# Performance work log

Hardware: AMD Instinct MI355X
Metric: run time of the kernel (lower is better)

Reference implementation:

```python
import jax, jax.numpy as jnp
import numpy as np
import math

HIDDEN = 32
N_NODES = 4096
N_EDGES = 8192
FEAT = HIDDEN * 16
# e3nn FullyConnectedTensorProduct instruction order: loop i_in1, i_in2, i_out
PATHS = [(l1, l2, l3) for l1 in range(4) for l2 in range(4) for l3 in range(4)
         if abs(l1 - l2) <= l3 <= l1 + l2 and (l1 + l2 + l3) % 2 == 0]
WEIGHT_NUMEL = len(PATHS) * HIDDEN * HIDDEN  # 23 * 1024 = 23552
_CNT = {l3: sum(1 for p in PATHS if p[2] == l3) for l3 in range(4)}
# path_weight: irrep_normalization='component', path_normalization='element'
PATH_W = {p: math.sqrt((2 * p[2] + 1) / (_CNT[p[2]] * HIDDEN)) for p in PATHS}


def _sh(xp, x, y, z):
    # e3nn-convention real spherical harmonics l=0..3, 'component' normalization.
    # Assumes unit-norm (x,y,z). xp is np or jnp.
    s3, s5, s7, s15 = math.sqrt(3.), math.sqrt(5.), math.sqrt(7.), math.sqrt(15.)
    c58, c38 = math.sqrt(5. / 8.), math.sqrt(3. / 8.)
    comps = [
        xp.ones_like(x),
        s3 * x, s3 * y, s3 * z,
        s5 * s3 * x * z, s5 * s3 * x * y, s5 * (y * y - 0.5 * (x * x + z * z)),
        s5 * s3 * y * z, s5 * (s3 / 2.) * (z * z - x * x),
        s7 * c58 * x * (3. * z * z - x * x), s7 * s15 * x * y * z,
        s7 * c38 * x * (5. * y * y - 1.), s7 * 0.5 * y * (5. * y * y - 3.),
        s7 * c38 * z * (5. * y * y - 1.), s7 * (s15 / 2.) * y * (z * z - x * x),
        s7 * c58 * z * (z * z - 3. * x * x),
    ]
    return xp.stack(comps, axis=-1)


def _wigner_tables():
    # Real-basis unit-Frobenius invariant tensors (e3nn wigner_3j up to sign),
    # computed as Gaunt integrals of the real SH over the sphere (exact quadrature:
    # integrand degree <= 9, Gauss-Legendre x uniform phi).
    nu, nphi = 16, 32
    u, wu = np.polynomial.legendre.leggauss(nu)
    phi = np.arange(nphi) * (2.0 * np.pi / nphi)
    uu = np.repeat(u, nphi)
    ww = np.repeat(wu, nphi) * (2.0 * np.pi / nphi)
    pp = np.tile(phi, nu)
    st = np.sqrt(np.maximum(1.0 - uu * uu, 0.0))
    Y = _sh(np, st * np.cos(pp), st * np.sin(pp), uu)  # [P,16]
    tabs = {}
    for key in set(PATHS):
        l1, l2, l3 = key
        C = np.einsum('p,pi,pj,pk->ijk', ww,
                      Y[:, l1 * l1:(l1 + 1) ** 2],
                      Y[:, l2 * l2:(l2 + 1) ** 2],
                      Y[:, l3 * l3:(l3 + 1) ** 2])
        tabs[key] = (C / np.linalg.norm(C)).astype(np.float32)
    return tabs


W3J = _wigner_tables()


def setup_inputs():
    key = jax.random.key(0)
    k1, k2, k3, k4, k5 = jax.random.split(key, 5)
    return {
        'node_features': jax.random.normal(k1, (N_NODES, FEAT), jnp.float32),
        'edge_index': jax.random.randint(k2, (2, N_EDGES), 0, N_NODES),
        'edge_vectors': jax.random.normal(k3, (N_EDGES, 3), jnp.float32),
        'w_weight': jax.random.uniform(k4, (WEIGHT_NUMEL, 1), jnp.float32, -1.0, 1.0),
        'w_bias': jax.random.uniform(k5, (WEIGHT_NUMEL,), jnp.float32, -1.0, 1.0),
    }


def reference(node_features, edge_index, edge_vectors, w_weight, w_bias):
    src, dst = edge_index[0], edge_index[1]
    N = node_features.shape[0]
    E = edge_vectors.shape[0]
    lengths = jnp.maximum(jnp.linalg.norm(edge_vectors, axis=-1, keepdims=True), 1e-8)
    unit = edge_vectors / lengths
    Y = _sh(jnp, unit[:, 0], unit[:, 1], unit[:, 2])            # [E,16]
    # weight_net: Linear(1, weight_numel)
    W = lengths * w_weight[:, 0][None, :] + w_bias[None, :]     # [E,23552]
    x_src = node_features[src]                                  # [E,512] gather
    acc = [jnp.zeros((E, HIDDEN, 2 * l + 1), node_features.dtype) for l in range(4)]
    for p_idx, (l1, l2, l3) in enumerate(PATHS):
        x1 = x_src[:, HIDDEN * l1 * l1: HIDDEN * (l1 + 1) ** 2].reshape(E, HIDDEN, 2 * l1 + 1)
        y2 = Y[:, l2 * l2:(l2 + 1) ** 2]                        # [E,2l2+1]
        C = jnp.asarray(W3J[(l1, l2, l3)])                      # [2l1+1,2l2+1,2l3+1]
        wp = W[:, p_idx * HIDDEN * HIDDEN:(p_idx + 1) * HIDDEN * HIDDEN].reshape(E, HIDDEN, HIDDEN)
        tmp = jnp.einsum('eui,ej,ijk->euk', x1, y2, C)
        acc[l3] = acc[l3] + PATH_W[(l1, l2, l3)] * jnp.einsum('euk,euw->ewk', tmp, wp)
    messages = jnp.concatenate([a.reshape(E, -1) for a in acc], axis=-1)  # [E,512]
    return jax.ops.segment_sum(messages, dst, num_segments=N)
```

## Files before the change

kernel.cpp:

```cpp
#include <hip/hip_runtime.h>
#include <math.h>

#define N_PATHS 23
#define HIDDEN  32
#define N_NODES 4096
#define N_EDGES 8192
#define FEAT    512
#define BLK     128
#define ZERO_BLOCKS 256

#define WAVE_SYNC() asm volatile("s_waitcnt lgkmcnt(0)" ::: "memory")

typedef __attribute__((ext_vector_type(8)))  short bf16x8;
typedef __attribute__((ext_vector_type(16))) float f32x16;

constexpr int cL1[N_PATHS] = {0,0,0,0, 1,1,1,1,1,1, 2,2,2,2,2,2,2, 3,3,3,3,3,3};
constexpr int cL2[N_PATHS] = {0,1,2,3, 0,1,1,2,2,3, 0,1,1,2,2,3,3, 0,1,2,2,3,3};
constexpr int cCOFF[N_PATHS]= {0,1,10,35,84,93,102,147,192,297,402,427,472,577,602,727,832,1077,1126,1231,1336,1581,1630};
constexpr int cL3P[N_PATHS] = {0,5,13,21, 1,4,7,11,15,19, 2,6,9,10,14,18,22, 3,8,12,16,17,20};
constexpr int cL3S[5] = {0,4,10,17,23};
constexpr int cOFF3[4] = {0,32,128,288};
__device__ const int CNT_L3[4] = {4,6,7,6};
__device__ const int D_L3[N_PATHS] = {0,1,2,3, 1,0,2,1,3,2, 2,1,3,0,2,1,3, 3,2,1,3,0,2};

constexpr int zOff(int G, int pi) {
    int off = 0;
    for (int q = cL3S[G]; q < pi; ++q) off += (2*cL1[cL3P[q]]+1)*(2*G+1);
    return off;
}

__device__ const double GLX8[8] = {
    -0.96028985649753623168, -0.79666647741362673959, -0.52553240991632898582, -0.18343464249564980494,
     0.18343464249564980494,  0.52553240991632898582,  0.79666647741362673959,  0.96028985649753623168};
__device__ const double GLW8[8] = {
     0.10122853629037625915,  0.22238103445337447054,  0.31370664587788728734,  0.36268378337836198297,
     0.36268378337836198297,  0.31370664587788728734,  0.22238103445337447054,  0.10122853629037625915};
__device__ const double COSP16[16] = {
  1.0,                     0.92387953251128675613,  0.70710678118654752440,  0.38268343236508977173,
  0.0,                    -0.38268343236508977173, -0.70710678118654752440, -0.92387953251128675613,
 -1.0,                    -0.92387953251128675613, -0.70710678118654752440, -0.38268343236508977173,
  0.0,                     0.38268343236508977173,  0.70710678118654752440,  0.92387953251128675613};
__device__ const double SINP16[16] = {
  0.0,                     0.38268343236508977173,  0.70710678118654752440,  0.92387953251128675613,
  1.0,                     0.92387953251128675613,  0.70710678118654752440,  0.38268343236508977173,
  0.0,                    -0.38268343236508977173, -0.70710678118654752440, -0.92387953251128675613,
 -1.0,                    -0.92387953251128675613, -0.70710678118654752440, -0.38268343236508977173};

__device__ inline void sh_f64(double x, double y, double z, double* Y) {
    const double s3 = 1.7320508075688772935, s5 = 2.2360679774997896964,
                 s7 = 2.6457513110645905905, s15 = 3.8729833462074168852;
    const double c58 = 0.79056941504209483300, c38 = 0.61237243569579452455;
    Y[0] = 1.0;
    Y[1] = s3*x;  Y[2] = s3*y;  Y[3] = s3*z;
    Y[4] = s5*s3*x*z;  Y[5] = s5*s3*x*y;
    Y[6] = s5*(y*y - 0.5*(x*x + z*z));
    Y[7] = s5*s3*y*z;  Y[8] = s5*(s3/2.0)*(z*z - x*x);
    Y[9] = s7*c58*x*(3.0*z*z - x*x);
    Y[10]= s7*s15*x*y*z;
    Y[11]= s7*c38*x*(5.0*y*y - 1.0);
    Y[12]= s7*0.5*y*(5.0*y*y - 3.0);
    Y[13]= s7*c38*z*(5.0*y*y - 1.0);
    Y[14]= s7*(s15/2.0)*y*(z*z - x*x);
// ... 88 lines not shown
        float acc = 0.f;
        if (entry < csize) {
            const int i = entry/(d2*d3); const int r = entry - i*(d2*d3);
            const int j = r/d3; const int k = r - j*d3;
            const int ai = l1*l1+i, bi = l2*l2+j, ci = l3*l3+k;
#pragma unroll 4
            for (int it = 0; it < 32; ++it) {
                const int q = it*4 + sub;
                acc = fmaf(s_wq[q] * s_Yq[q][ai] * s_Yq[q][bi], s_Yq[q][ci], acc);
            }
        }
        acc += __shfl_xor(acc, 1);
        acc += __shfl_xor(acc, 2);
        if (sub == 0 && entry < csize) s_part[entry] = acc;
    }
    __syncthreads();

    if (t < 256) { const float v = (t < csize) ? s_part[t] : 0.f; red[t] = v*v; }
    __syncthreads();
    for (int s = 128; s > 0; s >>= 1) {
        if (t < s) red[t] += red[t+s];
        __syncthreads();
    }
    if (t == 0) {
        const float pw = sqrtf((float)(2*l3+1) / ((float)CNT_L3[l3] * (float)HIDDEN));
        s_scale = pw / sqrtf(red[0]);
    }
    __syncthreads();
    if (t < csize) g_w3j[cCOFF[p] + t] = s_part[t] * s_scale;
}

template<int G, int P, int ZOFF>
__device__ __forceinline__ void do_zpath(
    int lane, const float* __restrict__ w3j, const float* sY, float* sz)
{
    constexpr int l1 = cL1[P], l2 = cL2[P];
    constexpr int d1 = 2*l1+1, d2 = 2*l2+1, d3 = 2*G+1;
    constexpr int zc = d1*d3;
#pragma unroll
    for (int base = 0; base < 4*zc; base += 64) {
        const int idx = base + lane;
        if (idx < 4*zc) {
            const int elz = idx / zc;
            const int r = idx - elz*zc;
            const int i = r / d3, k = r - i*d3;
            const float* Cp = w3j + cCOFF[P] + i*(d2*d3) + k;
            const float* Yp = sY + elz*16 + l2*l2;
            float acc = 0.f;
#pragma unroll
            for (int j = 0; j < d2; ++j) acc = fmaf(Yp[j], Cp[j*d3], acc);
            sz[4*ZOFF + elz*zc + r] = acc;
        }
    }
}

template<int G, int P, int ZOFF>
__device__ __forceinline__ void do_path(
    int lane, int el4, int u0, int bvaddr, int avaddr,
    const float (&xr0)[16], const float (&xr1)[16],
    const unsigned short* __restrict__ Awhi, const unsigned short* __restrict__ Awlo,
    const unsigned short* __restrict__ Abhi, const unsigned short* __restrict__ Ablo,
    const float* sz,
    unsigned short* sbh, unsigned short* sbl,
    f32x16 &Cw, f32x16 &Cb)
{
    constexpr int l1 = cL1[P];
    constexpr int d1 = 2*l1+1, d3 = 2*G+1;
    constexpr int zc = d1*d3;
    constexpr int xo = l1*l1;

    const unsigned short* pwh = Awhi + P*1024;
    const unsigned short* pwl = Awlo + P*1024;
    const unsigned short* pbh = Abhi + P*1024;
    const unsigned short* pbl = Ablo + P*1024;
    bf16x8 awh[2], awl[2], abh[2], abl[2];
#pragma unroll
    for (int kc = 0; kc < 2; ++kc) {
        awh[kc] = *(const bf16x8*)(pwh + avaddr + kc*16);
        awl[kc] = *(const bf16x8*)(pwl + avaddr + kc*16);
        abh[kc] = *(const bf16x8*)(pbh + avaddr + kc*16);
        abl[kc] = *(const bf16x8*)(pbl + avaddr + kc*16);
    }

    {
        const float* zr = sz + 4*ZOFF + el4*zc;
        unsigned short* bh = sbh + (el4*d3)*40 + 2*u0;
        unsigned short* bl = sbl + (el4*d3)*40 + 2*u0;
#pragma unroll
        for (int k = 0; k < d3; ++k) {
            float t0 = 0.f, t1 = 0.f;
#pragma unroll
            for (int i = 0; i < d1; ++i) {
                const float zz = zr[i*d3 + k];
                t0 = fmaf(xr0[xo+i], zz, t0);
                t1 = fmaf(xr1[xo+i], zz, t1);
            }
            const unsigned int b0 = __float_as_uint(t0);
            const unsigned int b1 = __float_as_uint(t1);
            const float l0 = t0 - __uint_as_float(b0 & 0xFFFF0000u);
            const float l1f = t1 - __uint_as_float(b1 & 0xFFFF0000u);
            *(unsigned int*)(bh + k*40) = (b0 >> 16) | (b1 & 0xFFFF0000u);
            *(unsigned int*)(bl + k*40) = (__float_as_uint(l0) >> 16) | (__float_as_uint(l1f) & 0xFFFF0000u);
        }
    }
    WAVE_SYNC();

#pragma unroll
    for (int kc = 0; kc < 2; ++kc) {
        const bf16x8 bh = *(const bf16x8*)(sbh + bvaddr + kc*16);
        const bf16x8 bl = *(const bf16x8*)(sbl + bvaddr + kc*16);
        Cw = __builtin_amdgcn_mfma_f32_32x32x16_bf16(awh[kc], bh, Cw, 0, 0, 0);
        Cb = __builtin_amdgcn_mfma_f32_32x32x16_bf16(abh[kc], bh, Cb, 0, 0, 0);
        Cw = __builtin_amdgcn_mfma_f32_32x32x16_bf16(awh[kc], bl, Cw, 0, 0, 0);
        Cb = __builtin_amdgcn_mfma_f32_32x32x16_bf16(abh[kc], bl, Cb, 0, 0, 0);
        Cw = __builtin_amdgcn_mfma_f32_32x32x16_bf16(awl[kc], bh, Cw, 0, 0, 0);
        Cb = __builtin_amdgcn_mfma_f32_32x32x16_bf16(abl[kc], bh, Cb, 0, 0, 0);
    }
    WAVE_SYNC();
}

template<int G>
__device__ __forceinline__ void do_group(
    int lane, int el4, int u0, int bvaddr, int avaddr,
    const float (&xr0)[16], const float (&xr1)[16],
    const float* __restrict__ w3j,
    const unsigned short* __restrict__ Awhi, const unsigned short* __restrict__ Awlo,
    const unsigned short* __restrict__ Abhi, const unsigned short* __restrict__ Ablo,
    const float* sY, float* sz,
    unsigned short* sbh, unsigned short* sbl,
    const float* slen, float* smsg)
{
    constexpr int d3 = 2*G+1;
    constexpr int s = cL3S[G];
    constexpr int n = cL3S[G+1] - cL3S[G];
    f32x16 Cw = (f32x16)(0.f), Cb = (f32x16)(0.f);

    do_zpath<G, cL3P[s+0], zOff(G,s+0)>(lane, w3j, sY, sz);
    do_zpath<G, cL3P[s+1], zOff(G,s+1)>(lane, w3j, sY, sz);
    do_zpath<G, cL3P[s+2], zOff(G,s+2)>(lane, w3j, sY, sz);
    do_zpath<G, cL3P[s+3], zOff(G,s+3)>(lane, w3j, sY, sz);
    if constexpr (n > 4) do_zpath<G, cL3P[s+4], zOff(G,s+4)>(lane, w3j, sY, sz);
    if constexpr (n > 5) do_zpath<G, cL3P[s+5], zOff(G,s+5)>(lane, w3j, sY, sz);
    if constexpr (n > 6) do_zpath<G, cL3P[s+6], zOff(G,s+6)>(lane, w3j, sY, sz);
    WAVE_SYNC();

    do_path<G, cL3P[s+0], zOff(G,s+0)>(lane,el4,u0,bvaddr,avaddr,xr0,xr1,Awhi,Awlo,Abhi,Ablo,sz,sbh,sbl,Cw,Cb);
    do_path<G, cL3P[s+1], zOff(G,s+1)>(lane,el4,u0,bvaddr,avaddr,xr0,xr1,Awhi,Awlo,Abhi,Ablo,sz,sbh,sbl,Cw,Cb);
    do_path<G, cL3P[s+2], zOff(G,s+2)>(lane,el4,u0,bvaddr,avaddr,xr0,xr1,Awhi,Awlo,Abhi,Ablo,sz,sbh,sbl,Cw,Cb);
    do_path<G, cL3P[s+3], zOff(G,s+3)>(lane,el4,u0,bvaddr,avaddr,xr0,xr1,Awhi,Awlo,Abhi,Ablo,sz,sbh,sbl,Cw,Cb);
    if constexpr (n > 4)
        do_path<G, cL3P[s+4], zOff(G,s+4)>(lane,el4,u0,bvaddr,avaddr,xr0,xr1,Awhi,Awlo,Abhi,Ablo,sz,sbh,sbl,Cw,Cb);
    if constexpr (n > 5)
        do_path<G, cL3P[s+5], zOff(G,s+5)>(lane,el4,u0,bvaddr,avaddr,xr0,xr1,Awhi,Awlo,Abhi,Ablo,sz,sbh,sbl,Cw,Cb);
    if constexpr (n > 6)
        do_path<G, cL3P[s+6], zOff(G,s+6)>(lane,el4,u0,bvaddr,avaddr,xr0,xr1,Awhi,Awlo,Abhi,Ablo,sz,sbh,sbl,Cw,Cb);

    const int col = lane & 31;
    if (col < 4*d3) {
        const int elc = col / d3, k = col - elc*d3;
        const float len = slen[elc];
        float* mp = smsg + elc*FEAT + cOFF3[G] + k;
#pragma unroll
        for (int reg = 0; reg < 16; ++reg) {
            const int w = (reg & 3) + 8*(reg >> 2) + 4*(lane >> 5);
            mp[w*d3] = fmaf(len, Cw[reg], Cb[reg]);
        }
    }
}

__global__ __launch_bounds__(BLK) void edge_kernel(
    const float* __restrict__ nf,
    const int*   __restrict__ eidx,
    const float* __restrict__ ev,
    const float* __restrict__ w3j,
    const unsigned short* __restrict__ Awhi,
    const unsigned short* __restrict__ Awlo,
    const unsigned short* __restrict__ Abhi,
    const unsigned short* __restrict__ Ablo,
    float*       __restrict__ out)
{
    __shared__ float s_zp[2][784];
    __shared__ float s_Y[2][64];
    __shared__ float s_len[2][4];
    __shared__ int   s_src[2][4];
    __shared__ int   s_dst[2][4];
    __shared__ __align__(16) unsigned short s_Bhi[2][1280];
    __shared__ __align__(16) unsigned short s_Blo[2][1280];
    __shared__ float s_msg[2][4*FEAT];

    const int t    = threadIdx.x;
    const int wave = t >> 6;
    const int lane = t & 63;
    const int el4  = lane >> 4;
    const int u0   = lane & 15;
    const int e0   = blockIdx.x * 8 + wave*4;
    const int bvaddr = (lane & 31)*40 + (lane >> 5)*8;
    const int avaddr = (lane & 31)*32 + (lane >> 5)*8;

    if (lane < 4) {
        const int e = e0 + lane;
        s_src[wave][lane] = eidx[e];
        s_dst[wave][lane] = eidx[N_EDGES + e];
        const float x = ev[e*3+0], y = ev[e*3+1], z = ev[e*3+2];
        const float len = sqrtf(x*x + y*y + z*z);
        const float lc = fmaxf(len, 1e-8f);
        s_len[wave][lane] = lc;
        float Yl[16];
        sh_f32(x/lc, y/lc, z/lc, Yl);
#pragma unroll
        for (int i = 0; i < 16; ++i) s_Y[wave][lane*16+i] = Yl[i];
    }
    WAVE_SYNC();

    float xr0[16], xr1[16];
    {
        const float* xrow = nf + (size_t)s_src[wave][el4]*FEAT;
        const int ua = 2*u0, ub = 2*u0 + 1;
        xr0[0] = xrow[ua];                 xr1[0] = xrow[ub];
#pragma unroll
        for (int i = 0; i < 3; ++i) { xr0[1+i] = xrow[32 + ua*3 + i];  xr1[1+i] = xrow[32 + ub*3 + i]; }
#pragma unroll
        for (int i = 0; i < 5; ++i) { xr0[4+i] = xrow[128 + ua*5 + i]; xr1[4+i] = xrow[128 + ub*5 + i]; }
#pragma unroll
        for (int i = 0; i < 7; ++i) { xr0[9+i] = xrow[288 + ua*7 + i]; xr1[9+i] = xrow[288 + ub*7 + i]; }
    }

    do_group<0>(lane,el4,u0,bvaddr,avaddr,xr0,xr1,w3j,Awhi,Awlo,Abhi,Ablo,
                s_Y[wave], s_zp[wave], s_Bhi[wave], s_Blo[wave], s_len[wave], s_msg[wave]);
    do_group<1>(lane,el4,u0,bvaddr,avaddr,xr0,xr1,w3j,Awhi,Awlo,Abhi,Ablo,
                s_Y[wave], s_zp[wave], s_Bhi[wave], s_Blo[wave], s_len[wave], s_msg[wave]);
    do_group<2>(lane,el4,u0,bvaddr,avaddr,xr0,xr1,w3j,Awhi,Awlo,Abhi,Ablo,
                s_Y[wave], s_zp[wave], s_Bhi[wave], s_Blo[wave], s_len[wave], s_msg[wave]);
    do_group<3>(lane,el4,u0,bvaddr,avaddr,xr0,xr1,w3j,Awhi,Awlo,Abhi,Ablo,
                s_Y[wave], s_zp[wave], s_Bhi[wave], s_Blo[wave], s_len[wave], s_msg[wave]);
    WAVE_SYNC();

    for (int i = lane; i < 4*FEAT; i += 64) {
        const int elc = i >> 9, m = i & 511;
        atomicAdd(&out[(size_t)s_dst[wave][elc]*FEAT + m], s_msg[wave][i]);
    }
}

extern "C" void kernel_launch(void* const* d_in, const int* in_sizes, int n_in,
                              void* d_out, int out_size, void* d_ws, size_t ws_size,
                              hipStream_t stream) {
    const float* nf   = (const float*)d_in[0];
    const int*   eidx = (const int*)  d_in[1];
    const float* ev   = (const float*)d_in[2];
    const float* ww   = (const float*)d_in[3];
    const float* wb   = (const float*)d_in[4];
    float* out = (float*)d_out;

    float* w3j = (float*)d_ws;
    unsigned short* Awhi = (unsigned short*)((char*)d_ws + 16384);
    unsigned short* Awlo = Awhi + N_PATHS*1024;
    unsigned short* Abhi = Awlo + N_PATHS*1024;
    unsigned short* Ablo = Abhi + N_PATHS*1024;

    w3j_setup_kernel<<<N_PATHS + ZERO_BLOCKS, 512, 0, stream>>>(
        ww, wb, w3j, Awhi, Awlo, Abhi, Ablo, out);
    edge_kernel<<<N_EDGES/8, BLK, 0, stream>>>(nf, eidx, ev, w3j, Awhi, Awlo, Abhi, Ablo, out);
}
```

Baseline: 122.2 us.

## Split each edge quartet's paths across two waves with shared-memory accumulation

Each block now handles 4 edges instead of 8, and the two waves split the 23 tensor-product paths between them. The split is a fixed balanced assignment per output irrep, so each wave handles a subset of paths for the same edges. Partial messages from both waves are combined in shared memory with atomic adds, then flushed to global memory with atomics. This doubles the grid size and shortens each wave's serial path chain to expose more parallelism. The cost is shared-memory zeroing, LDS atomics, block barriers, and twice as many blocks each redundantly loading the same node rows and spherical harmonics.

New measurement: 153.9 us. +26.0%, slower.

```diff
diff --git a/kernel.cpp b/kernel.cpp
--- a/kernel.cpp
+++ b/kernel.cpp
@@ -23,9 +23,16 @@
 __device__ const int CNT_L3[4] = {4,6,7,6};
 __device__ const int D_L3[N_PATHS] = {0,1,2,3, 1,0,2,1,3,2, 2,1,3,0,2,1,3, 3,2,1,3,0,2};
 
-constexpr int zOff(int G, int pi) {
+constexpr int SUBN[4][2] = {{2,2},{3,3},{4,3},{2,4}};
+constexpr int SUBS[4][2][4] = {
+  {{0,3,-1,-1},   {1,2,-1,-1}},
+  {{4,5,9,-1},    {6,7,8,-1}},
+  {{10,11,13,15}, {12,14,16,-1}},
+  {{21,22,-1,-1}, {17,18,19,20}},
+};
+constexpr int subZOff(int G, int W, int i) {
     int off = 0;
-    for (int q = cL3S[G]; q < pi; ++q) off += (2*cL1[cL3P[q]]+1)*(2*G+1);
+    for (int q = 0; q < i; ++q) off += (2*cL1[cL3P[SUBS[G][W][q]]]+1)*(2*G+1);
     return off;
 }
 
@@ -269,7 +276,7 @@
     WAVE_SYNC();
 }
 
-template<int G>
+template<int G, int W>
 __device__ __forceinline__ void do_group(
     int lane, int el4, int u0, int bvaddr, int avaddr,
     const float (&xr0)[16], const float (&xr1)[16],
@@ -281,29 +288,25 @@
     const float* slen, float* smsg)
 {
     constexpr int d3 = 2*G+1;
-    constexpr int s = cL3S[G];
-    constexpr int n = cL3S[G+1] - cL3S[G];
+    constexpr int n  = SUBN[G][W];
+    constexpr int sA = SUBS[G][W][0];
+    constexpr int sB = SUBS[G][W][1];
+    constexpr int sC = (SUBS[G][W][2] < 0) ? sA : SUBS[G][W][2];
+    constexpr int sD = (SUBS[G][W][3] < 0) ? sA : SUBS[G][W][3];
     f32x16 Cw = (f32x16)(0.f), Cb = (f32x16)(0.f);
 
-    do_zpath<G, cL3P[s+0], zOff(G,s+0)>(lane, w3j, sY, sz);
-    do_zpath<G, cL3P[s+1], zOff(G,s+1)>(lane, w3j, sY, sz);
-    do_zpath<G, cL3P[s+2], zOff(G,s+2)>(lane, w3j, sY, sz);
-    do_zpath<G, cL3P[s+3], zOff(G,s+3)>(lane, w3j, sY, sz);
-    if constexpr (n > 4) do_zpath<G, cL3P[s+4], zOff(G,s+4)>(lane, w3j, sY, sz);
-    if constexpr (n > 5) do_zpath<G, cL3P[s+5], zOff(G,s+5)>(lane, w3j, sY, sz);
-    if constexpr (n > 6) do_zpath<G, cL3P[s+6], zOff(G,s+6)>(lane, w3j, sY, sz);
+    do_zpath<G, cL3P[sA], subZOff(G,W,0)>(lane, w3j, sY, sz);
+    do_zpath<G, cL3P[sB], subZOff(G,W,1)>(lane, w3j, sY, sz);
+    if constexpr (n > 2) do_zpath<G, cL3P[sC], subZOff(G,W,2)>(lane, w3j, sY, sz);
+    if constexpr (n > 3) do_zpath<G, cL3P[sD], subZOff(G,W,3)>(lane, w3j, sY, sz);
     WAVE_SYNC();
 
-    do_path<G, cL3P[s+0], zOff(G,s+0)>(lane,el4,u0,bvaddr,avaddr,xr0,xr1,Awhi,Awlo,Abhi,Ablo,sz,sbh,sbl,Cw,Cb);
-    do_path<G, cL3P[s+1], zOff(G,s+1)>(lane,el4,u0,bvaddr,avaddr,xr0,xr1,Awhi,Awlo,Abhi,Ablo,sz,sbh,sbl,Cw,Cb);
-    do_path<G, cL3P[s+2], zOff(G,s+2)>(lane,el4,u0,bvaddr,avaddr,xr0,xr1,Awhi,Awlo,Abhi,Ablo,sz,sbh,sbl,Cw,Cb);
-    do_path<G, cL3P[s+3], zOff(G,s+3)>(lane,el4,u0,bvaddr,avaddr,xr0,xr1,Awhi,Awlo,Abhi,Ablo,sz,sbh,sbl,Cw,Cb);
-    if constexpr (n > 4)
-        do_path<G, cL3P[s+4], zOff(G,s+4)>(lane,el4,u0,bvaddr,avaddr,xr0,xr1,Awhi,Awlo,Abhi,Ablo,sz,sbh,sbl,Cw,Cb);
-    if constexpr (n > 5)
-        do_path<G, cL3P[s+5], zOff(G,s+5)>(lane,el4,u0,bvaddr,avaddr,xr0,xr1,Awhi,Awlo,Abhi,Ablo,sz,sbh,sbl,Cw,Cb);
-    if constexpr (n > 6)
-        do_path<G, cL3P[s+6], zOff(G,s+6)>(lane,el4,u0,bvaddr,avaddr,xr0,xr1,Awhi,Awlo,Abhi,Ablo,sz,sbh,sbl,Cw,Cb);
+    do_path<G, cL3P[sA], subZOff(G,W,0)>(lane,el4,u0,bvaddr,avaddr,xr0,xr1,Awhi,Awlo,Abhi,Ablo,sz,sbh,sbl,Cw,Cb);
+    do_path<G, cL3P[sB], subZOff(G,W,1)>(lane,el4,u0,bvaddr,avaddr,xr0,xr1,Awhi,Awlo,Abhi,Ablo,sz,sbh,sbl,Cw,Cb);
+    if constexpr (n > 2)
+        do_path<G, cL3P[sC], subZOff(G,W,2)>(lane,el4,u0,bvaddr,avaddr,xr0,xr1,Awhi,Awlo,Abhi,Ablo,sz,sbh,sbl,Cw,Cb);
+    if constexpr (n > 3)
+        do_path<G, cL3P[sD], subZOff(G,W,3)>(lane,el4,u0,bvaddr,avaddr,xr0,xr1,Awhi,Awlo,Abhi,Ablo,sz,sbh,sbl,Cw,Cb);
 
     const int col = lane & 31;
     if (col < 4*d3) {
@@ -313,7 +316,7 @@
 #pragma unroll
         for (int reg = 0; reg < 16; ++reg) {
             const int w = (reg & 3) + 8*(reg >> 2) + 4*(lane >> 5);
-            mp[w*d3] = fmaf(len, Cw[reg], Cb[reg]);
+            atomicAdd(&mp[w*d3], fmaf(len, Cw[reg], Cb[reg]));
         }
     }
 }
@@ -329,42 +332,43 @@
     const unsigned short* __restrict__ Ablo,
     float*       __restrict__ out)
 {
-    __shared__ float s_zp[2][784];
-    __shared__ float s_Y[2][64];
-    __shared__ float s_len[2][4];
-    __shared__ int   s_src[2][4];
-    __shared__ int   s_dst[2][4];
+    __shared__ float s_zp[2][392];
+    __shared__ float s_Y[64];
+    __shared__ float s_len[4];
+    __shared__ int   s_src[4];
+    __shared__ int   s_dst[4];
     __shared__ __align__(16) unsigned short s_Bhi[2][1280];
     __shared__ __align__(16) unsigned short s_Blo[2][1280];
-    __shared__ float s_msg[2][4*FEAT];
+    __shared__ float s_msg[4*FEAT];
 
     const int t    = threadIdx.x;
     const int wave = t >> 6;
     const int lane = t & 63;
     const int el4  = lane >> 4;
     const int u0   = lane & 15;
-    const int e0   = blockIdx.x * 8 + wave*4;
+    const int e0   = blockIdx.x * 4;
     const int bvaddr = (lane & 31)*40 + (lane >> 5)*8;
     const int avaddr = (lane & 31)*32 + (lane >> 5)*8;
 
-    if (lane < 4) {
-        const int e = e0 + lane;
-        s_src[wave][lane] = eidx[e];
-        s_dst[wave][lane] = eidx[N_EDGES + e];
+    if (t < 4) {
+        const int e = e0 + t;
+        s_src[t] = eidx[e];
+        s_dst[t] = eidx[N_EDGES + e];
         const float x = ev[e*3+0], y = ev[e*3+1], z = ev[e*3+2];
         const float len = sqrtf(x*x + y*y + z*z);
         const float lc = fmaxf(len, 1e-8f);
-        s_len[wave][lane] = lc;
+        s_len[t] = lc;
         float Yl[16];
         sh_f32(x/lc, y/lc, z/lc, Yl);
 #pragma unroll
-        for (int i = 0; i < 16; ++i) s_Y[wave][lane*16+i] = Yl[i];
-    }
-    WAVE_SYNC();
+        for (int i = 0; i < 16; ++i) s_Y[t*16+i] = Yl[i];
+    }
+    for (int i = t; i < 4*FEAT; i += BLK) s_msg[i] = 0.f;
+    __syncthreads();
 
     float xr0[16], xr1[16];
     {
-        const float* xrow = nf + (size_t)s_src[wave][el4]*FEAT;
+        const float* xrow = nf + (size_t)s_src[el4]*FEAT;
         const int ua = 2*u0, ub = 2*u0 + 1;
         xr0[0] = xrow[ua];                 xr1[0] = xrow[ub];
 #pragma unroll
@@ -375,19 +379,30 @@
         for (int i = 0; i < 7; ++i) { xr0[9+i] = xrow[288 + ua*7 + i]; xr1[9+i] = xrow[288 + ub*7 + i]; }
     }
 
-    do_group<0>(lane,el4,u0,bvaddr,avaddr,xr0,xr1,w3j,Awhi,Awlo,Abhi,Ablo,
-                s_Y[wave], s_zp[wave], s_Bhi[wave], s_Blo[wave], s_len[wave], s_msg[wave]);
-    do_group<1>(lane,el4,u0,bvaddr,avaddr,xr0,xr1,w3j,Awhi,Awlo,Abhi,Ablo,
-                s_Y[wave], s_zp[wave], s_Bhi[wave], s_Blo[wave], s_len[wave], s_msg[wave]);
-    do_group<2>(lane,el4,u0,bvaddr,avaddr,xr0,xr1,w3j,Awhi,Awlo,Abhi,Ablo,
-                s_Y[wave], s_zp[wave], s_Bhi[wave], s_Blo[wave], s_len[wave], s_msg[wave]);
-    do_group<3>(lane,el4,u0,bvaddr,avaddr,xr0,xr1,w3j,Awhi,Awlo,Abhi,Ablo,
-                s_Y[wave], s_zp[wave], s_Bhi[wave], s_Blo[wave], s_len[wave], s_msg[wave]);
-    WAVE_SYNC();
-
-    for (int i = lane; i < 4*FEAT; i += 64) {
+    if (wave == 0) {
+        do_group<0,0>(lane,el4,u0,bvaddr,avaddr,xr0,xr1,w3j,Awhi,Awlo,Abhi,Ablo,
+                      s_Y, s_zp[0], s_Bhi[0], s_Blo[0], s_len, s_msg);
+        do_group<1,0>(lane,el4,u0,bvaddr,avaddr,xr0,xr1,w3j,Awhi,Awlo,Abhi,Ablo,
+                      s_Y, s_zp[0], s_Bhi[0], s_Blo[0], s_len, s_msg);
+        do_group<2,0>(lane,el4,u0,bvaddr,avaddr,xr0,xr1,w3j,Awhi,Awlo,Abhi,Ablo,
+                      s_Y, s_zp[0], s_Bhi[0], s_Blo[0], s_len, s_msg);
+        do_group<3,0>(lane,el4,u0,bvaddr,avaddr,xr0,xr1,w3j,Awhi,Awlo,Abhi,Ablo,
+                      s_Y, s_zp[0], s_Bhi[0], s_Blo[0], s_len, s_msg);
+    } else {
+        do_group<0,1>(lane,el4,u0,bvaddr,avaddr,xr0,xr1,w3j,Awhi,Awlo,Abhi,Ablo,
+                      s_Y, s_zp[1], s_Bhi[1], s_Blo[1], s_len, s_msg);
+        do_group<1,1>(lane,el4,u0,bvaddr,avaddr,xr0,xr1,w3j,Awhi,Awlo,Abhi,Ablo,
+                      s_Y, s_zp[1], s_Bhi[1], s_Blo[1], s_len, s_msg);
+        do_group<2,1>(lane,el4,u0,bvaddr,avaddr,xr0,xr1,w3j,Awhi,Awlo,Abhi,Ablo,
+                      s_Y, s_zp[1], s_Bhi[1], s_Blo[1], s_len, s_msg);
+        do_group<3,1>(lane,el4,u0,bvaddr,avaddr,xr0,xr1,w3j,Awhi,Awlo,Abhi,Ablo,
+                      s_Y, s_zp[1], s_Bhi[1], s_Blo[1], s_len, s_msg);
+    }
+    __syncthreads();
+
+    for (int i = t; i < 4*FEAT; i += BLK) {
         const int elc = i >> 9, m = i & 511;
-        atomicAdd(&out[(size_t)s_dst[wave][elc]*FEAT + m], s_msg[wave][i]);
+        atomicAdd(&out[(size_t)s_dst[elc]*FEAT + m], s_msg[i]);
     }
 }
 
@@ -409,5 +424,5 @@
 
     w3j_setup_kernel<<<N_PATHS + ZERO_BLOCKS, 512, 0, stream>>>(
         ww, wb, w3j, Awhi, Awlo, Abhi, Ablo, out);
-    edge_kernel<<<N_EDGES/8, BLK, 0, stream>>>(nf, eidx, ev, w3j, Awhi, Awlo, Abhi, Ablo, out);
-}
+    edge_kernel<<<N_EDGES/4, BLK, 0, stream>>>(nf, eidx, ev, w3j, Awhi, Awlo, Abhi, Ablo, out);
+}
```

## Split K dimension across two waves per 4-edge group and atomically write MFMA outputs

Applied to the files above, without the earlier changes.

Each block now processes 4 edges instead of 8, and its two waves split the 32 input channels (K dimension) between them. Each wave runs one MFMA K-chunk per path instead of two, and the z-path precompute is shared across both waves with block-level syncs. The shared-memory message staging buffer is removed: each wave atomically adds its partial results directly into the output. This doubles the grid, lowers per-wave register use and shared memory, and adds parallelism, at the cost of twice as many global atomics and extra __syncthreads.

Result: slower. 207.1 us (+69.5%).

```diff
diff --git a/kernel.cpp b/kernel.cpp
--- a/kernel.cpp
+++ b/kernel.cpp
@@ -28,6 +28,8 @@
     for (int q = cL3S[G]; q < pi; ++q) off += (2*cL1[cL3P[q]]+1)*(2*G+1);
     return off;
 }
+
+#define BSTR 24
 
 __device__ const double GLX8[8] = {
     -0.96028985649753623168, -0.79666647741362673959, -0.52553240991632898582, -0.18343464249564980494,
@@ -182,14 +184,14 @@
 
 template<int G, int P, int ZOFF>
 __device__ __forceinline__ void do_zpath(
-    int lane, const float* __restrict__ w3j, const float* sY, float* sz)
+    int t, const float* __restrict__ w3j, const float* sY, float* sz)
 {
     constexpr int l1 = cL1[P], l2 = cL2[P];
     constexpr int d1 = 2*l1+1, d2 = 2*l2+1, d3 = 2*G+1;
     constexpr int zc = d1*d3;
 #pragma unroll
-    for (int base = 0; base < 4*zc; base += 64) {
-        const int idx = base + lane;
+    for (int base = 0; base < 4*zc; base += 128) {
+        const int idx = base + t;
         if (idx < 4*zc) {
             const int elz = idx / zc;
             const int r = idx - elz*zc;
@@ -206,8 +208,8 @@
 
 template<int G, int P, int ZOFF>
 __device__ __forceinline__ void do_path(
-    int lane, int el4, int u0, int bvaddr, int avaddr,
-    const float (&xr0)[16], const float (&xr1)[16],
+    int lane, int el4, int ul, int bvaddr, int avaddr,
+    const float (&xr)[16],
     const unsigned short* __restrict__ Awhi, const unsigned short* __restrict__ Awlo,
     const unsigned short* __restrict__ Abhi, const unsigned short* __restrict__ Ablo,
     const float* sz,
@@ -223,99 +225,88 @@
     const unsigned short* pwl = Awlo + P*1024;
     const unsigned short* pbh = Abhi + P*1024;
     const unsigned short* pbl = Ablo + P*1024;
-    bf16x8 awh[2], awl[2], abh[2], abl[2];
-#pragma unroll
-    for (int kc = 0; kc < 2; ++kc) {
-        awh[kc] = *(const bf16x8*)(pwh + avaddr + kc*16);
-        awl[kc] = *(const bf16x8*)(pwl + avaddr + kc*16);
-        abh[kc] = *(const bf16x8*)(pbh + avaddr + kc*16);
-        abl[kc] = *(const bf16x8*)(pbl + avaddr + kc*16);
-    }
+    const bf16x8 awh = *(const bf16x8*)(pwh + avaddr);
+    const bf16x8 awl = *(const bf16x8*)(pwl + avaddr);
+    const bf16x8 abh = *(const bf16x8*)(pbh + avaddr);
+    const bf16x8 abl = *(const bf16x8*)(pbl + avaddr);
 
     {
         const float* zr = sz + 4*ZOFF + el4*zc;
-        unsigned short* bh = sbh + (el4*d3)*40 + 2*u0;
-        unsigned short* bl = sbl + (el4*d3)*40 + 2*u0;
+        unsigned short* bh = sbh + (el4*d3)*BSTR + ul;
+        unsigned short* bl = sbl + (el4*d3)*BSTR + ul;
 #pragma unroll
         for (int k = 0; k < d3; ++k) {
-            float t0 = 0.f, t1 = 0.f;
-#pragma unroll
-            for (int i = 0; i < d1; ++i) {
-                const float zz = zr[i*d3 + k];
-                t0 = fmaf(xr0[xo+i], zz, t0);
-                t1 = fmaf(xr1[xo+i], zz, t1);
-            }
+            float t0 = 0.f;
+#pragma unroll
+            for (int i = 0; i < d1; ++i)
+                t0 = fmaf(xr[xo+i], zr[i*d3 + k], t0);
             const unsigned int b0 = __float_as_uint(t0);
-            const unsigned int b1 = __float_as_uint(t1);
             const float l0 = t0 - __uint_as_float(b0 & 0xFFFF0000u);
-            const float l1f = t1 - __uint_as_float(b1 & 0xFFFF0000u);
-            *(unsigned int*)(bh + k*40) = (b0 >> 16) | (b1 & 0xFFFF0000u);
-            *(unsigned int*)(bl + k*40) = (__float_as_uint(l0) >> 16) | (__float_as_uint(l1f) & 0xFFFF0000u);
+            bh[k*BSTR] = (unsigned short)(b0 >> 16);
+            bl[k*BSTR] = (unsigned short)(__float_as_uint(l0) >> 16);
         }
     }
     WAVE_SYNC();
 
-#pragma unroll
-    for (int kc = 0; kc < 2; ++kc) {
-        const bf16x8 bh = *(const bf16x8*)(sbh + bvaddr + kc*16);
-        const bf16x8 bl = *(const bf16x8*)(sbl + bvaddr + kc*16);
-        Cw = __builtin_amdgcn_mfma_f32_32x32x16_bf16(awh[kc], bh, Cw, 0, 0, 0);
-        Cb = __builtin_amdgcn_mfma_f32_32x32x16_bf16(abh[kc], bh, Cb, 0, 0, 0);
-        Cw = __builtin_amdgcn_mfma_f32_32x32x16_bf16(awh[kc], bl, Cw, 0, 0, 0);
-        Cb = __builtin_amdgcn_mfma_f32_32x32x16_bf16(abh[kc], bl, Cb, 0, 0, 0);
-        Cw = __builtin_amdgcn_mfma_f32_32x32x16_bf16(awl[kc], bh, Cw, 0, 0, 0);
-        Cb = __builtin_amdgcn_mfma_f32_32x32x16_bf16(abl[kc], bh, Cb, 0, 0, 0);
-    }
+    const bf16x8 bhv = *(const bf16x8*)(sbh + bvaddr);
+    const bf16x8 blv = *(const bf16x8*)(sbl + bvaddr);
+    Cw = __builtin_amdgcn_mfma_f32_32x32x16_bf16(awh, bhv, Cw, 0, 0, 0);
+    Cb = __builtin_amdgcn_mfma_f32_32x32x16_bf16(abh, bhv, Cb, 0, 0, 0);
+    Cw = __builtin_amdgcn_mfma_f32_32x32x16_bf16(awh, blv, Cw, 0, 0, 0);
+    Cb = __builtin_amdgcn_mfma_f32_32x32x16_bf16(abh, blv, Cb, 0, 0, 0);
+    Cw = __builtin_amdgcn_mfma_f32_32x32x16_bf16(awl, bhv, Cw, 0, 0, 0);
+    Cb = __builtin_amdgcn_mfma_f32_32x32x16_bf16(abl, bhv, Cb, 0, 0, 0);
     WAVE_SYNC();
 }
 
 template<int G>
 __device__ __forceinline__ void do_group(
-    int lane, int el4, int u0, int bvaddr, int avaddr,
-    const float (&xr0)[16], const float (&xr1)[16],
+    int t, int lane, int el4, int ul, int bvaddr, int avaddr,
+    const float (&xr)[16],
     const float* __restrict__ w3j,
     const unsigned short* __restrict__ Awhi, const unsigned short* __restrict__ Awlo,
     const unsigned short* __restrict__ Abhi, const unsigned short* __restrict__ Ablo,
     const float* sY, float* sz,
     unsigned short* sbh, unsigned short* sbl,
-    const float* slen, float* smsg)
+    const float* slen, const int* sdst, float* __restrict__ out)
 {
     constexpr int d3 = 2*G+1;
     constexpr int s = cL3S[G];
     constexpr int n = cL3S[G+1] - cL3S[G];
     f32x16 Cw = (f32x16)(0.f), Cb = (f32x16)(0.f);
 
-    do_zpath<G, cL3P[s+0], zOff(G,s+0)>(lane, w3j, sY, sz);
-    do_zpath<G, cL3P[s+1], zOff(G,s+1)>(lane, w3j, sY, sz);
-    do_zpath<G, cL3P[s+2], zOff(G,s+2)>(lane, w3j, sY, sz);
-    do_zpath<G, cL3P[s+3], zOff(G,s+3)>(lane, w3j, sY, sz);
-    if constexpr (n > 4) do_zpath<G, cL3P[s+4], zOff(G,s+4)>(lane, w3j, sY, sz);
-    if constexpr (n > 5) do_zpath<G, cL3P[s+5], zOff(G,s+5)>(lane, w3j, sY, sz);
-    if constexpr (n > 6) do_zpath<G, cL3P[s+6], zOff(G,s+6)>(lane, w3j, sY, sz);
-    WAVE_SYNC();
-
-    do_path<G, cL3P[s+0], zOff(G,s+0)>(lane,el4,u0,bvaddr,avaddr,xr0,xr1,Awhi,Awlo,Abhi,Ablo,sz,sbh,sbl,Cw,Cb);
-    do_path<G, cL3P[s+1], zOff(G,s+1)>(lane,el4,u0,bvaddr,avaddr,xr0,xr1,Awhi,Awlo,Abhi,Ablo,sz,sbh,sbl,Cw,Cb);
-    do_path<G, cL3P[s+2], zOff(G,s+2)>(lane,el4,u0,bvaddr,avaddr,xr0,xr1,Awhi,Awlo,Abhi,Ablo,sz,sbh,sbl,Cw,Cb);
-    do_path<G, cL3P[s+3], zOff(G,s+3)>(lane,el4,u0,bvaddr,avaddr,xr0,xr1,Awhi,Awlo,Abhi,Ablo,sz,sbh,sbl,Cw,Cb);
+    do_zpath<G, cL3P[s+0], zOff(G,s+0)>(t, w3j, sY, sz);
+    do_zpath<G, cL3P[s+1], zOff(G,s+1)>(t, w3j, sY, sz);
+    do_zpath<G, cL3P[s+2], zOff(G,s+2)>(t, w3j, sY, sz);
+    do_zpath<G, cL3P[s+3], zOff(G,s+3)>(t, w3j, sY, sz);
+    if constexpr (n > 4) do_zpath<G, cL3P[s+4], zOff(G,s+4)>(t, w3j, sY, sz);
+    if constexpr (n > 5) do_zpath<G, cL3P[s+5], zOff(G,s+5)>(t, w3j, sY, sz);
+    if constexpr (n > 6) do_zpath<G, cL3P[s+6], zOff(G,s+6)>(t, w3j, sY, sz);
+    __syncthreads();
+
+    do_path<G, cL3P[s+0], zOff(G,s+0)>(lane,el4,ul,bvaddr,avaddr,xr,Awhi,Awlo,Abhi,Ablo,sz,sbh,sbl,Cw,Cb);
+    do_path<G, cL3P[s+1], zOff(G,s+1)>(lane,el4,ul,bvaddr,avaddr,xr,Awhi,Awlo,Abhi,Ablo,sz,sbh,sbl,Cw,Cb);
+    do_path<G, cL3P[s+2], zOff(G,s+2)>(lane,el4,ul,bvaddr,avaddr,xr,Awhi,Awlo,Abhi,Ablo,sz,sbh,sbl,Cw,Cb);
+    do_path<G, cL3P[s+3], zOff(G,s+3)>(lane,el4,ul,bvaddr,avaddr,xr,Awhi,Awlo,Abhi,Ablo,sz,sbh,sbl,Cw,Cb);
     if constexpr (n > 4)
-        do_path<G, cL3P[s+4], zOff(G,s+4)>(lane,el4,u0,bvaddr,avaddr,xr0,xr1,Awhi,Awlo,Abhi,Ablo,sz,sbh,sbl,Cw,Cb);
+        do_path<G, cL3P[s+4], zOff(G,s+4)>(lane,el4,ul,bvaddr,avaddr,xr,Awhi,Awlo,Abhi,Ablo,sz,sbh,sbl,Cw,Cb);
     if constexpr (n > 5)
-        do_path<G, cL3P[s+5], zOff(G,s+5)>(lane,el4,u0,bvaddr,avaddr,xr0,xr1,Awhi,Awlo,Abhi,Ablo,sz,sbh,sbl,Cw,Cb);
+        do_path<G, cL3P[s+5], zOff(G,s+5)>(lane,el4,ul,bvaddr,avaddr,xr,Awhi,Awlo,Abhi,Ablo,sz,sbh,sbl,Cw,Cb);
     if constexpr (n > 6)
-        do_path<G, cL3P[s+6], zOff(G,s+6)>(lane,el4,u0,bvaddr,avaddr,xr0,xr1,Awhi,Awlo,Abhi,Ablo,sz,sbh,sbl,Cw,Cb);
+        do_path<G, cL3P[s+6], zOff(G,s+6)>(lane,el4,ul,bvaddr,avaddr,xr,Awhi,Awlo,Abhi,Ablo,sz,sbh,sbl,Cw,Cb);
 
     const int col = lane & 31;
     if (col < 4*d3) {
         const int elc = col / d3, k = col - elc*d3;
         const float len = slen[elc];
-        float* mp = smsg + elc*FEAT + cOFF3[G] + k;
+        float* op = out + (size_t)sdst[elc]*FEAT + cOFF3[G] + k;
 #pragma unroll
         for (int reg = 0; reg < 16; ++reg) {
             const int w = (reg & 3) + 8*(reg >> 2) + 4*(lane >> 5);
-            mp[w*d3] = fmaf(len, Cw[reg], Cb[reg]);
+            atomicAdd(&op[w*d3], fmaf(len, Cw[reg], Cb[reg]));
         }
     }
+    __syncthreads();
 }
 
 __global__ __launch_bounds__(BLK) void edge_kernel(
@@ -329,66 +320,59 @@
     const unsigned short* __restrict__ Ablo,
     float*       __restrict__ out)
 {
-    __shared__ float s_zp[2][784];
-    __shared__ float s_Y[2][64];
-    __shared__ float s_len[2][4];
-    __shared__ int   s_src[2][4];
-    __shared__ int   s_dst[2][4];
-    __shared__ __align__(16) unsigned short s_Bhi[2][1280];
-    __shared__ __align__(16) unsigned short s_Blo[2][1280];
-    __shared__ float s_msg[2][4*FEAT];
+    __shared__ float s_zp[784];
+    __shared__ float s_Y[64];
+    __shared__ float s_len[4];
+    __shared__ int   s_src[4];
+    __shared__ int   s_dst[4];
+    __shared__ __align__(16) unsigned short s_Bhi[2][32*BSTR];
+    __shared__ __align__(16) unsigned short s_Blo[2][32*BSTR];
 
     const int t    = threadIdx.x;
     const int wave = t >> 6;
     const int lane = t & 63;
     const int el4  = lane >> 4;
-    const int u0   = lane & 15;
-    const int e0   = blockIdx.x * 8 + wave*4;
-    const int bvaddr = (lane & 31)*40 + (lane >> 5)*8;
-    const int avaddr = (lane & 31)*32 + (lane >> 5)*8;
-
-    if (lane < 4) {
-        const int e = e0 + lane;
-        s_src[wave][lane] = eidx[e];
-        s_dst[wave][lane] = eidx[N_EDGES + e];
+    const int ul   = lane & 15;
+    const int e0   = blockIdx.x * 4;
+    const int bvaddr = (lane & 31)*BSTR + (lane >> 5)*8;
+    const int avaddr = (lane & 31)*32 + 16*wave + (lane >> 5)*8;
+
+    if (t < 4) {
+        const int e = e0 + t;
+        s_src[t] = eidx[e];
+        s_dst[t] = eidx[N_EDGES + e];
         const float x = ev[e*3+0], y = ev[e*3+1], z = ev[e*3+2];
         const float len = sqrtf(x*x + y*y + z*z);
         const float lc = fmaxf(len, 1e-8f);
-        s_len[wave][lane] = lc;
+        s_len[t] = lc;
         float Yl[16];
         sh_f32(x/lc, y/lc, z/lc, Yl);
 #pragma unroll
-        for (int i = 0; i < 16; ++i) s_Y[wave][lane*16+i] = Yl[i];
-    }
-    WAVE_SYNC();
-
-    float xr0[16], xr1[16];
+        for (int i = 0; i < 16; ++i) s_Y[t*16+i] = Yl[i];
+    }
+    __syncthreads();
+
+    float xr[16];
     {
-        const float* xrow = nf + (size_t)s_src[wave][el4]*FEAT;
-        const int ua = 2*u0, ub = 2*u0 + 1;
-        xr0[0] = xrow[ua];                 xr1[0] = xrow[ub];
-#pragma unroll
-        for (int i = 0; i < 3; ++i) { xr0[1+i] = xrow[32 + ua*3 + i];  xr1[1+i] = xrow[32 + ub*3 + i]; }
-#pragma unroll
-        for (int i = 0; i < 5; ++i) { xr0[4+i] = xrow[128 + ua*5 + i]; xr1[4+i] = xrow[128 + ub*5 + i]; }
-#pragma unroll
-        for (int i = 0; i < 7; ++i) { xr0[9+i] = xrow[288 + ua*7 + i]; xr1[9+i] = xrow[288 + ub*7 + i]; }
-    }
-
-    do_group<0>(lane,el4,u0,bvaddr,avaddr,xr0,xr1,w3j,Awhi,Awlo,Abhi,Ablo,
-                s_Y[wave], s_zp[wave], s_Bhi[wave], s_Blo[wave], s_len[wave], s_msg[wave]);
-    do_group<1>(lane,el4,u0,bvaddr,avaddr,xr0,xr1,w3j,Awhi,Awlo,Abhi,Ablo,
-                s_Y[wave], s_zp[wave], s_Bhi[wave], s_Blo[wave], s_len[wave], s_msg[wave]);
-    do_group<2>(lane,el4,u0,bvaddr,avaddr,xr0,xr1,w3j,Awhi,Awlo,Abhi,Ablo,
-                s_Y[wave], s_zp[wave], s_Bhi[wave], s_Blo[wave], s_len[wave], s_msg[wave]);
-    do_group<3>(lane,el4,u0,bvaddr,avaddr,xr0,xr1,w3j,Awhi,Awlo,Abhi,Ablo,
-                s_Y[wave], s_zp[wave], s_Bhi[wave], s_Blo[wave], s_len[wave], s_msg[wave]);
-    WAVE_SYNC();
-
-    for (int i = lane; i < 4*FEAT; i += 64) {
-        const int elc = i >> 9, m = i & 511;
-        atomicAdd(&out[(size_t)s_dst[wave][elc]*FEAT + m], s_msg[wave][i]);
-    }
+        const float* xrow = nf + (size_t)s_src[el4]*FEAT;
+        const int u = 16*wave + ul;
+        xr[0] = xrow[u];
+#pragma unroll
+        for (int i = 0; i < 3; ++i) xr[1+i] = xrow[32 + u*3 + i];
+#pragma unroll
+        for (int i = 0; i < 5; ++i) xr[4+i] = xrow[128 + u*5 + i];
+#pragma unroll
+        for (int i = 0; i < 7; ++i) xr[9+i] = xrow[288 + u*7 + i];
+    }
+
+    do_group<0>(t,lane,el4,ul,bvaddr,avaddr,xr,w3j,Awhi,Awlo,Abhi,Ablo,
+                s_Y, s_zp, s_Bhi[wave], s_Blo[wave], s_len, s_dst, out);
+    do_group<1>(t,lane,el4,ul,bvaddr,avaddr,xr,w3j,Awhi,Awlo,Abhi,Ablo,
+                s_Y, s_zp, s_Bhi[wave], s_Blo[wave], s_len, s_dst, out);
+    do_group<2>(t,lane,el4,ul,bvaddr,avaddr,xr,w3j,Awhi,Awlo,Abhi,Ablo,
+                s_Y, s_zp, s_Bhi[wave], s_Blo[wave], s_len, s_dst, out);
+    do_group<3>(t,lane,el4,ul,bvaddr,avaddr,xr,w3j,Awhi,Awlo,Abhi,Ablo,
+                s_Y, s_zp, s_Bhi[wave], s_Blo[wave], s_len, s_dst, out);
 }
 
 extern "C" void kernel_launch(void* const* d_in, const int* in_sizes, int n_in,
@@ -409,5 +393,5 @@
 
     w3j_setup_kernel<<<N_PATHS + ZERO_BLOCKS, 512, 0, stream>>>(
         ww, wb, w3j, Awhi, Awlo, Abhi, Ablo, out);
-    edge_kernel<<<N_EDGES/8, BLK, 0, stream>>>(nf, eidx, ev, w3j, Awhi, Awlo, Abhi, Ablo, out);
-}
+    edge_kernel<<<N_EDGES/4, BLK, 0, stream>>>(nf, eidx, ev, w3j, Awhi, Awlo, Abhi, Ablo, out);
+}
```

## Process two edges per single-wave block instead of four per wave

Applied to the files above, without the earlier changes.

Each wave now handles 2 edges instead of 4, with one lane per hidden channel rather than two, and blocks shrink to one wave with four times as many blocks launched. The aim is more wavefronts in flight, fewer registers per lane and less serial per-lane work for latency hiding. In exchange, the 32x32 MFMA tile carries only 2*d3 useful columns, so total MFMA work and per-edge weight-fragment loads roughly double. B-tile writes also become 16-bit stores instead of 32-bit.

New measurement: 146.4 us. 19.8% more time.

```diff
diff --git a/kernel.cpp b/kernel.cpp
--- a/kernel.cpp
+++ b/kernel.cpp
@@ -6,7 +6,7 @@
 #define N_NODES 4096
 #define N_EDGES 8192
 #define FEAT    512
-#define BLK     128
+#define BLK     64
 #define ZERO_BLOCKS 256
 
 #define WAVE_SYNC() asm volatile("s_waitcnt lgkmcnt(0)" ::: "memory")
@@ -188,9 +188,9 @@
     constexpr int d1 = 2*l1+1, d2 = 2*l2+1, d3 = 2*G+1;
     constexpr int zc = d1*d3;
 #pragma unroll
-    for (int base = 0; base < 4*zc; base += 64) {
+    for (int base = 0; base < 2*zc; base += 64) {
         const int idx = base + lane;
-        if (idx < 4*zc) {
+        if (idx < 2*zc) {
             const int elz = idx / zc;
             const int r = idx - elz*zc;
             const int i = r / d3, k = r - i*d3;
@@ -199,15 +199,15 @@
             float acc = 0.f;
 #pragma unroll
             for (int j = 0; j < d2; ++j) acc = fmaf(Yp[j], Cp[j*d3], acc);
-            sz[4*ZOFF + elz*zc + r] = acc;
+            sz[2*ZOFF + elz*zc + r] = acc;
         }
     }
 }
 
 template<int G, int P, int ZOFF>
 __device__ __forceinline__ void do_path(
-    int lane, int el4, int u0, int bvaddr, int avaddr,
-    const float (&xr0)[16], const float (&xr1)[16],
+    int lane, int el, int ul, int bvaddr, int avaddr,
+    const float (&xr)[16],
     const unsigned short* __restrict__ Awhi, const unsigned short* __restrict__ Awlo,
     const unsigned short* __restrict__ Abhi, const unsigned short* __restrict__ Ablo,
     const float* sz,
@@ -233,24 +233,19 @@
     }
 
     {
-        const float* zr = sz + 4*ZOFF + el4*zc;
-        unsigned short* bh = sbh + (el4*d3)*40 + 2*u0;
-        unsigned short* bl = sbl + (el4*d3)*40 + 2*u0;
+        const float* zr = sz + 2*ZOFF + el*zc;
+        unsigned short* bh = sbh + (el*d3)*40 + ul;
+        unsigned short* bl = sbl + (el*d3)*40 + ul;
 #pragma unroll
         for (int k = 0; k < d3; ++k) {
-            float t0 = 0.f, t1 = 0.f;
-#pragma unroll
-            for (int i = 0; i < d1; ++i) {
-                const float zz = zr[i*d3 + k];
-                t0 = fmaf(xr0[xo+i], zz, t0);
-                t1 = fmaf(xr1[xo+i], zz, t1);
-            }
+            float t0 = 0.f;
+#pragma unroll
+            for (int i = 0; i < d1; ++i)
+                t0 = fmaf(xr[xo+i], zr[i*d3 + k], t0);
             const unsigned int b0 = __float_as_uint(t0);
-            const unsigned int b1 = __float_as_uint(t1);
             const float l0 = t0 - __uint_as_float(b0 & 0xFFFF0000u);
-            const float l1f = t1 - __uint_as_float(b1 & 0xFFFF0000u);
-            *(unsigned int*)(bh + k*40) = (b0 >> 16) | (b1 & 0xFFFF0000u);
-            *(unsigned int*)(bl + k*40) = (__float_as_uint(l0) >> 16) | (__float_as_uint(l1f) & 0xFFFF0000u);
+            bh[k*40] = (unsigned short)(b0 >> 16);
+            bl[k*40] = (unsigned short)(__float_as_uint(l0) >> 16);
         }
     }
     WAVE_SYNC();
@@ -271,8 +266,8 @@
 
 template<int G>
 __device__ __forceinline__ void do_group(
-    int lane, int el4, int u0, int bvaddr, int avaddr,
-    const float (&xr0)[16], const float (&xr1)[16],
+    int lane, int el, int ul, int bvaddr, int avaddr,
+    const float (&xr)[16],
     const float* __restrict__ w3j,
     const unsigned short* __restrict__ Awhi, const unsigned short* __restrict__ Awlo,
     const unsigned short* __restrict__ Abhi, const unsigned short* __restrict__ Ablo,
@@ -294,19 +289,19 @@
     if constexpr (n > 6) do_zpath<G, cL3P[s+6], zOff(G,s+6)>(lane, w3j, sY, sz);
     WAVE_SYNC();
 
-    do_path<G, cL3P[s+0], zOff(G,s+0)>(lane,el4,u0,bvaddr,avaddr,xr0,xr1,Awhi,Awlo,Abhi,Ablo,sz,sbh,sbl,Cw,Cb);
-    do_path<G, cL3P[s+1], zOff(G,s+1)>(lane,el4,u0,bvaddr,avaddr,xr0,xr1,Awhi,Awlo,Abhi,Ablo,sz,sbh,sbl,Cw,Cb);
-    do_path<G, cL3P[s+2], zOff(G,s+2)>(lane,el4,u0,bvaddr,avaddr,xr0,xr1,Awhi,Awlo,Abhi,Ablo,sz,sbh,sbl,Cw,Cb);
-    do_path<G, cL3P[s+3], zOff(G,s+3)>(lane,el4,u0,bvaddr,avaddr,xr0,xr1,Awhi,Awlo,Abhi,Ablo,sz,sbh,sbl,Cw,Cb);
+    do_path<G, cL3P[s+0], zOff(G,s+0)>(lane,el,ul,bvaddr,avaddr,xr,Awhi,Awlo,Abhi,Ablo,sz,sbh,sbl,Cw,Cb);
+    do_path<G, cL3P[s+1], zOff(G,s+1)>(lane,el,ul,bvaddr,avaddr,xr,Awhi,Awlo,Abhi,Ablo,sz,sbh,sbl,Cw,Cb);
+    do_path<G, cL3P[s+2], zOff(G,s+2)>(lane,el,ul,bvaddr,avaddr,xr,Awhi,Awlo,Abhi,Ablo,sz,sbh,sbl,Cw,Cb);
+    do_path<G, cL3P[s+3], zOff(G,s+3)>(lane,el,ul,bvaddr,avaddr,xr,Awhi,Awlo,Abhi,Ablo,sz,sbh,sbl,Cw,Cb);
     if constexpr (n > 4)
-        do_path<G, cL3P[s+4], zOff(G,s+4)>(lane,el4,u0,bvaddr,avaddr,xr0,xr1,Awhi,Awlo,Abhi,Ablo,sz,sbh,sbl,Cw,Cb);
+        do_path<G, cL3P[s+4], zOff(G,s+4)>(lane,el,ul,bvaddr,avaddr,xr,Awhi,Awlo,Abhi,Ablo,sz,sbh,sbl,Cw,Cb);
     if constexpr (n > 5)
-        do_path<G, cL3P[s+5], zOff(G,s+5)>(lane,el4,u0,bvaddr,avaddr,xr0,xr1,Awhi,Awlo,Abhi,Ablo,sz,sbh,sbl,Cw,Cb);
+        do_path<G, cL3P[s+5], zOff(G,s+5)>(lane,el,ul,bvaddr,avaddr,xr,Awhi,Awlo,Abhi,Ablo,sz,sbh,sbl,Cw,Cb);
     if constexpr (n > 6)
-        do_path<G, cL3P[s+6], zOff(G,s+6)>(lane,el4,u0,bvaddr,avaddr,xr0,xr1,Awhi,Awlo,Abhi,Ablo,sz,sbh,sbl,Cw,Cb);
+        do_path<G, cL3P[s+6], zOff(G,s+6)>(lane,el,ul,bvaddr,avaddr,xr,Awhi,Awlo,Abhi,Ablo,sz,sbh,sbl,Cw,Cb);
 
     const int col = lane & 31;
-    if (col < 4*d3) {
+    if (col < 2*d3) {
         const int elc = col / d3, k = col - elc*d3;
         const float len = slen[elc];
         float* mp = smsg + elc*FEAT + cOFF3[G] + k;
@@ -329,65 +324,63 @@
     const unsigned short* __restrict__ Ablo,
     float*       __restrict__ out)
 {
-    __shared__ float s_zp[2][784];
-    __shared__ float s_Y[2][64];
-    __shared__ float s_len[2][4];
-    __shared__ int   s_src[2][4];
-    __shared__ int   s_dst[2][4];
-    __shared__ __align__(16) unsigned short s_Bhi[2][1280];
-    __shared__ __align__(16) unsigned short s_Blo[2][1280];
-    __shared__ float s_msg[2][4*FEAT];
-
-    const int t    = threadIdx.x;
-    const int wave = t >> 6;
-    const int lane = t & 63;
-    const int el4  = lane >> 4;
-    const int u0   = lane & 15;
-    const int e0   = blockIdx.x * 8 + wave*4;
+    __shared__ float s_zp[392];
+    __shared__ float s_Y[32];
+    __shared__ float s_len[2];
+    __shared__ int   s_src[2];
+    __shared__ int   s_dst[2];
+    __shared__ __align__(16) unsigned short s_Bhi[1280];
+    __shared__ __align__(16) unsigned short s_Blo[1280];
+    __shared__ float s_msg[2*FEAT];
+
+    const int lane = threadIdx.x;
+    const int el   = lane >> 5;
+    const int ul   = lane & 31;
+    const int e0   = blockIdx.x * 2;
     const int bvaddr = (lane & 31)*40 + (lane >> 5)*8;
     const int avaddr = (lane & 31)*32 + (lane >> 5)*8;
 
-    if (lane < 4) {
+    if (lane < 2) {
         const int e = e0 + lane;
-        s_src[wave][lane] = eidx[e];
-        s_dst[wave][lane] = eidx[N_EDGES + e];
+        s_src[lane] = eidx[e];
+        s_dst[lane] = eidx[N_EDGES + e];
         const float x = ev[e*3+0], y = ev[e*3+1], z = ev[e*3+2];
         const float len = sqrtf(x*x + y*y + z*z);
         const float lc = fmaxf(len, 1e-8f);
-        s_len[wave][lane] = lc;
+        s_len[lane] = lc;
         float Yl[16];
         sh_f32(x/lc, y/lc, z/lc, Yl);
 #pragma unroll
-        for (int i = 0; i < 16; ++i) s_Y[wave][lane*16+i] = Yl[i];
+        for (int i = 0; i < 16; ++i) s_Y[lane*16+i] = Yl[i];
     }
     WAVE_SYNC();
 
-    float xr0[16], xr1[16];
+    float xr[16];
     {
-        const float* xrow = nf + (size_t)s_src[wave][el4]*FEAT;
-        const int ua = 2*u0, ub = 2*u0 + 1;
-        xr0[0] = xrow[ua];                 xr1[0] = xrow[ub];
-#pragma unroll
-        for (int i = 0; i < 3; ++i) { xr0[1+i] = xrow[32 + ua*3 + i];  xr1[1+i] = xrow[32 + ub*3 + i]; }
-#pragma unroll
-        for (int i = 0; i < 5; ++i) { xr0[4+i] = xrow[128 + ua*5 + i]; xr1[4+i] = xrow[128 + ub*5 + i]; }
-#pragma unroll
-        for (int i = 0; i < 7; ++i) { xr0[9+i] = xrow[288 + ua*7 + i]; xr1[9+i] = xrow[288 + ub*7 + i]; }
-    }
-
-    do_group<0>(lane,el4,u0,bvaddr,avaddr,xr0,xr1,w3j,Awhi,Awlo,Abhi,Ablo,
-                s_Y[wave], s_zp[wave], s_Bhi[wave], s_Blo[wave], s_len[wave], s_msg[wave]);
-    do_group<1>(lane,el4,u0,bvaddr,avaddr,xr0,xr1,w3j,Awhi,Awlo,Abhi,Ablo,
-                s_Y[wave], s_zp[wave], s_Bhi[wave], s_Blo[wave], s_len[wave], s_msg[wave]);
-    do_group<2>(lane,el4,u0,bvaddr,avaddr,xr0,xr1,w3j,Awhi,Awlo,Abhi,Ablo,
-                s_Y[wave], s_zp[wave], s_Bhi[wave], s_Blo[wave], s_len[wave], s_msg[wave]);
-    do_group<3>(lane,el4,u0,bvaddr,avaddr,xr0,xr1,w3j,Awhi,Awlo,Abhi,Ablo,
-                s_Y[wave], s_zp[wave], s_Bhi[wave], s_Blo[wave], s_len[wave], s_msg[wave]);
+        const float* xrow = nf + (size_t)s_src[el]*FEAT;
+        const int u = ul;
+        xr[0] = xrow[u];
+#pragma unroll
+        for (int i = 0; i < 3; ++i) xr[1+i] = xrow[32 + u*3 + i];
+#pragma unroll
+        for (int i = 0; i < 5; ++i) xr[4+i] = xrow[128 + u*5 + i];
+#pragma unroll
+        for (int i = 0; i < 7; ++i) xr[9+i] = xrow[288 + u*7 + i];
+    }
+
+    do_group<0>(lane,el,ul,bvaddr,avaddr,xr,w3j,Awhi,Awlo,Abhi,Ablo,
+                s_Y, s_zp, s_Bhi, s_Blo, s_len, s_msg);
+    do_group<1>(lane,el,ul,bvaddr,avaddr,xr,w3j,Awhi,Awlo,Abhi,Ablo,
+                s_Y, s_zp, s_Bhi, s_Blo, s_len, s_msg);
+    do_group<2>(lane,el,ul,bvaddr,avaddr,xr,w3j,Awhi,Awlo,Abhi,Ablo,
+                s_Y, s_zp, s_Bhi, s_Blo, s_len, s_msg);
+    do_group<3>(lane,el,ul,bvaddr,avaddr,xr,w3j,Awhi,Awlo,Abhi,Ablo,
+                s_Y, s_zp, s_Bhi, s_Blo, s_len, s_msg);
     WAVE_SYNC();
 
-    for (int i = lane; i < 4*FEAT; i += 64) {
+    for (int i = lane; i < 2*FEAT; i += 64) {
         const int elc = i >> 9, m = i & 511;
-        atomicAdd(&out[(size_t)s_dst[wave][elc]*FEAT + m], s_msg[wave][i]);
+        atomicAdd(&out[(size_t)s_dst[elc]*FEAT + m], s_msg[i]);
     }
 }
 
@@ -409,5 +402,5 @@
 
     w3j_setup_kernel<<<N_PATHS + ZERO_BLOCKS, 512, 0, stream>>>(
         ww, wb, w3j, Awhi, Awlo, Abhi, Ablo, out);
-    edge_kernel<<<N_EDGES/8, BLK, 0, stream>>>(nf, eidx, ev, w3j, Awhi, Awlo, Abhi, Ablo, out);
-}
+    edge_kernel<<<N_EDGES/2, BLK, 0, stream>>>(nf, eidx, ev, w3j, Awhi, Awlo, Abhi, Ablo, out);
+}
```
